# Kernel optimization log

Hardware: AMD Instinct MI355X
Metric: run time of the kernel (lower is better)

## Reference

```python
import jax, jax.numpy as jnp
import numpy as np

N_NODES = 50000
N_EDGES = 800000
IN_DIM = 128
HID = 64
ZDIM = 64
N_GRAPHS = 64


def gcn_conv(x, W, b, src, dst, n):
    # PyG GCNConv: add self-loops, symmetric deg^-1/2 normalization,
    # linear transform then gather-scatter aggregation.
    h = x @ W  # [N, out]
    loops = jnp.arange(n, dtype=src.dtype)
    s = jnp.concatenate([src, loops])
    d = jnp.concatenate([dst, loops])
    deg = jnp.zeros((n,), h.dtype).at[d].add(1.0)  # includes self-loops -> >=1
    dinv = jax.lax.rsqrt(deg)
    norm = dinv[s] * dinv[d]  # [E+N]
    msg = h[s] * norm[:, None]  # gather [E+N, out]
    out = jnp.zeros_like(h).at[d].add(msg)  # scatter-add
    return out + b


def mean_pool(h, batch, num_graphs):
    sums = jax.ops.segment_sum(h, batch, num_segments=num_graphs)
    cnt = jax.ops.segment_sum(jnp.ones((h.shape[0],), h.dtype), batch,
                              num_segments=num_graphs)
    return sums / jnp.maximum(cnt, 1.0)[:, None]


def setup_inputs() -> dict:
    key = jax.random.key(0)
    ks = jax.random.split(key, 9)
    x = jax.random.normal(ks[0], (N_NODES, IN_DIM), jnp.float32)
    edge_index = jax.random.randint(ks[1], (2, N_EDGES), 0, N_NODES, jnp.int64 if jax.config.jax_enable_x64 else jnp.int32)
    batch = jnp.sort(jax.random.randint(ks[2], (N_NODES,), 0, N_GRAPHS))
    s1 = 1.0 / np.sqrt(IN_DIM)
    s2 = 1.0 / np.sqrt(HID)
    W1 = jax.random.uniform(ks[3], (IN_DIM, HID), jnp.float32, -s1, s1)
    b1 = jnp.zeros((HID,), jnp.float32)
    Wmu = jax.random.uniform(ks[4], (HID, ZDIM), jnp.float32, -s2, s2)
    bmu = jnp.zeros((ZDIM,), jnp.float32)
    Wsig = jax.random.uniform(ks[5], (HID, ZDIM), jnp.float32, -s2, s2)
    bsig = jnp.zeros((ZDIM,), jnp.float32)
    return {"x": x, "edge_index": edge_index, "batch": batch,
            "num_graphs": N_GRAPHS, "W1": W1, "b1": b1,
            "Wmu": Wmu, "bmu": bmu, "Wsig": Wsig, "bsig": bsig}


def reference(x, edge_index, batch, num_graphs, W1, b1, Wmu, bmu, Wsig, bsig):
    src, dst = edge_index[0], edge_index[1]
    n = x.shape[0]
    h = jax.nn.elu(gcn_conv(x, W1, b1, src, dst, n))
    z_mu = mean_pool(jax.nn.elu(gcn_conv(h, Wmu, bmu, src, dst, n)), batch, num_graphs)
    z_sigma = mean_pool(jax.nn.elu(gcn_conv(h, Wsig, bsig, src, dst, n)), batch, num_graphs)
    return (z_mu, z_sigma)
```

## Files before the change

kernel.cpp:

```cpp
#include <hip/hip_runtime.h>
#include <hip/hip_fp16.h>


#define IN_DIM 128
#define HID 64
#define ZDIM 64
#define N_GRAPHS 64
#define SCAN_B 1024
#define POOL2_WAVES 8192

__device__ __forceinline__ float elu1(float x) {
    return x > 0.f ? x : expm1f(x);
}

__global__ void k_count(const int* __restrict__ dst, int* __restrict__ kc,
                        int* __restrict__ rank, int E) {
    int e = blockIdx.x * blockDim.x + threadIdx.x;
    if (e < E) rank[e] = atomicAdd(&kc[dst[e]], 1);
}

__global__ __launch_bounds__(SCAN_B) void k_scan1(const int* __restrict__ kc,
                                                  int* __restrict__ bsum, int n) {
    __shared__ int wpart[16];
    int tid = threadIdx.x, lane = tid & 63, w = tid >> 6;
    int i = blockIdx.x * SCAN_B + tid;
    int v = (i < n) ? kc[i] : 0;
#pragma unroll
    for (int d = 1; d < 64; d <<= 1) v += __shfl_xor(v, d, 64);
    if (lane == 0) wpart[w] = v;
    __syncthreads();
    if (tid < 16) {
        int t = wpart[tid];
#pragma unroll
        for (int d = 1; d < 16; d <<= 1) t += __shfl_xor(t, d, 64);
        if (tid == 0) bsum[blockIdx.x] = t;
    }
}

__global__ __launch_bounds__(SCAN_B) void k_scan3(const int* __restrict__ kc,
                                                  const int* __restrict__ bsum,
                                                  int* __restrict__ offs,
                                                  float* __restrict__ dinv,
                                                  int n, int nb) {
    __shared__ int wsum[16];
    __shared__ int sbase;
    int tid = threadIdx.x, lane = tid & 63, w = tid >> 6;
    if (tid < 64) {
        int v = (tid < nb) ? bsum[tid] : 0;
        int s = v;
#pragma unroll
        for (int d = 1; d < 64; d <<= 1) {
            int u = __shfl_up(s, d, 64);
            if (tid >= d) s += u;
        }
        if (tid == blockIdx.x) sbase = s - v;
    }
    int i = blockIdx.x * SCAN_B + tid;
    int v = (i < n) ? kc[i] : 0;
    int s = v;
#pragma unroll
    for (int d = 1; d < 64; d <<= 1) {
        int u = __shfl_up(s, d, 64);
        if (lane >= d) s += u;
    }
    if (lane == 63) wsum[w] = s;
    __syncthreads();
    if (tid < 16) {
        int t = wsum[tid];
#pragma unroll
        for (int d = 1; d < 16; d <<= 1) {
            int u = __shfl_up(t, d, 64);
            if (tid >= d) t += u;
        }
        wsum[tid] = t;
    }
    __syncthreads();
    int base = sbase + ((w == 0) ? 0 : wsum[w - 1]);
    if (i < n) {
        offs[i + 1] = base + s;
        dinv[i] = 1.0f / sqrtf(1.0f + (float)v);
        if (i == 0) offs[0] = 0;
    }
}

__global__ void k_fill(const int* __restrict__ src, const int* __restrict__ dst,
                       const int* __restrict__ rank, const int* __restrict__ offs,
                       int* __restrict__ csr, int E) {
    int e = blockIdx.x * blockDim.x + threadIdx.x;
    if (e < E) csr[offs[dst[e]] + rank[e]] = src[e];
}

__global__ __launch_bounds__(256) void k_mm1(const float* __restrict__ x,
                                             const float* __restrict__ W,
                                             const float* __restrict__ dinv,
                                             __half* __restrict__ ts1h, int n) {
    __shared__ float xs[64 * 68];
    __shared__ float ws[64 * 68];
    const int tid = threadIdx.x;
    const int m0 = blockIdx.x * 64;
    const int j = tid & 15;
    const int i = tid >> 4;

    const float4* x4 = (const float4*)x;
    const float4* W4 = (const float4*)W;

    float4 acc[4];
#pragma unroll
    for (int r = 0; r < 4; ++r) acc[r] = make_float4(0.f, 0.f, 0.f, 0.f);

    for (int kk = 0; kk < IN_DIM; kk += 64) {
        __syncthreads();
        for (int idx = tid; idx < 64 * 16; idx += 256) {
            int row = idx >> 4, c4 = idx & 15;
            float4 v = make_float4(0.f, 0.f, 0.f, 0.f);
            if (m0 + row < n) v = x4[(size_t)(m0 + row) * 32 + (kk >> 2) + c4];
            *(float4*)&xs[row * 68 + 4 * c4] = v;
            *(float4*)&ws[row * 68 + 4 * c4] = W4[(size_t)(kk + row) * 16 + c4];
        }
        __syncthreads();
#pragma unroll 1
        for (int k4 = 0; k4 < 16; ++k4) {
            float4 a[4];
#pragma unroll
            for (int r = 0; r < 4; ++r)
                a[r] = *(const float4*)&xs[(4 * i + r) * 68 + 4 * k4];
#pragma unroll
            for (int kc = 0; kc < 4; ++kc) {
                float4 bv = *(const float4*)&ws[(4 * k4 + kc) * 68 + 4 * j];
#pragma unroll
                for (int r = 0; r < 4; ++r) {
                    float av = (&a[r].x)[kc];
                    acc[r].x = fmaf(av, bv.x, acc[r].x);
                    acc[r].y = fmaf(av, bv.y, acc[r].y);
                    acc[r].z = fmaf(av, bv.z, acc[r].z);
                    acc[r].w = fmaf(av, bv.w, acc[r].w);
                }
            }
        }
    }

#pragma unroll
    for (int r = 0; r < 4; ++r) {
        int row = m0 + 4 * i + r;
        if (row < n) {
            float di = dinv[row];
            float4 tv = acc[r];
            __half2* p = (__half2*)&ts1h[(size_t)row * HID + 4 * j];
            p[0] = __floats2half2_rn(tv.x * di, tv.y * di);
            p[1] = __floats2half2_rn(tv.z * di, tv.w * di);
        }
    }
}

__global__ __launch_bounds__(256) void k_gather_h(const int* __restrict__ off,
                                                  const int* __restrict__ csr,
                                                  const float* __restrict__ dinv,
                                                  const __half* __restrict__ ts,
                                                  float* __restrict__ out, int n) {
    int node = blockIdx.x * 4 + (threadIdx.x >> 6);
    if (node >= n) return;
    int lane = threadIdx.x & 63;
    int half = lane >> 5, l2 = lane & 31;
    int s0 = off[node], s1 = off[node + 1];
    float2 acc = make_float2(0.f, 0.f);
    int k = s0 + half;
    for (; k + 6 < s1; k += 8) {
        int a = csr[k], b = csr[k + 2], c = csr[k + 4], d = csr[k + 6];
        float2 fa = __half22float2(*(const __half2*)&ts[(size_t)a * 64 + 2 * l2]);
        float2 fb = __half22float2(*(const __half2*)&ts[(size_t)b * 64 + 2 * l2]);
        float2 fc = __half22float2(*(const __half2*)&ts[(size_t)c * 64 + 2 * l2]);
        float2 fd = __half22float2(*(const __half2*)&ts[(size_t)d * 64 + 2 * l2]);
        acc.x += (fa.x + fb.x) + (fc.x + fd.x);
        acc.y += (fa.y + fb.y) + (fc.y + fd.y);
    }
    for (; k + 2 < s1; k += 4) {
        int a = csr[k], b = csr[k + 2];
        float2 fa = __half22float2(*(const __half2*)&ts[(size_t)a * 64 + 2 * l2]);
        float2 fb = __half22float2(*(const __half2*)&ts[(size_t)b * 64 + 2 * l2]);
        acc.x += fa.x + fb.x;
        acc.y += fa.y + fb.y;
    }
    for (; k < s1; k += 2) {
        int a = csr[k];
        float2 fa = __half22float2(*(const __half2*)&ts[(size_t)a * 64 + 2 * l2]);
        acc.x += fa.x;
        acc.y += fa.y;
    }
    acc.x += __shfl_xor(acc.x, 32, 64);
    acc.y += __shfl_xor(acc.y, 32, 64);
    if (half == 0) {
        float2 self = __half22float2(*(const __half2*)&ts[(size_t)node * 64 + 2 * l2]);
        float di = dinv[node];
        float2 o = make_float2((acc.x + self.x) * di, (acc.y + self.y) * di);
        *(float2*)&out[(size_t)node * 64 + 2 * l2] = o;
    }
}

__global__ __launch_bounds__(256) void k_mm23(const float* __restrict__ agg1,
                                              const float* __restrict__ b1,
                                              const float* __restrict__ Wmu,
                                              const float* __restrict__ Wsig,
                                              const float* __restrict__ dinv,
                                              __half* __restrict__ CDh, int n) {
    __shared__ float hs[64 * 68];
    __shared__ float wc[64 * 132];
    const int tid = threadIdx.x;
    const int m0 = blockIdx.x * 64;
    const int j = tid & 15;
    const int i = tid >> 4;

    const float4* h4 = (const float4*)agg1;
    const float4* b14 = (const float4*)b1;
    const float4* Wm4 = (const float4*)Wmu;
    const float4* Ws4 = (const float4*)Wsig;
    for (int idx = tid; idx < 64 * 16; idx += 256) {
        int row = idx >> 4, c4 = idx & 15;
        float4 v = make_float4(0.f, 0.f, 0.f, 0.f);
        if (m0 + row < n) {
            float4 hv = h4[(size_t)(m0 + row) * 16 + c4];
            float4 bb = b14[c4];
            v.x = elu1(hv.x + bb.x);
            v.y = elu1(hv.y + bb.y);
            v.z = elu1(hv.z + bb.z);
            v.w = elu1(hv.w + bb.w);
        }
        *(float4*)&hs[row * 68 + 4 * c4] = v;
        *(float4*)&wc[row * 132 + 4 * c4] = Wm4[(size_t)row * 16 + c4];
        *(float4*)&wc[row * 132 + 64 + 4 * c4] = Ws4[(size_t)row * 16 + c4];
    }
    __syncthreads();

    float4 accm[4], accs[4];
#pragma unroll
    for (int r = 0; r < 4; ++r) {
        accm[r] = make_float4(0.f, 0.f, 0.f, 0.f);
        accs[r] = make_float4(0.f, 0.f, 0.f, 0.f);
    }

#pragma unroll 1
    for (int k4 = 0; k4 < 16; ++k4) {
        float4 a[4];
#pragma unroll
        for (int r = 0; r < 4; ++r)
            a[r] = *(const float4*)&hs[(4 * i + r) * 68 + 4 * k4];
#pragma unroll
        for (int kc = 0; kc < 4; ++kc) {
            float4 bm = *(const float4*)&wc[(4 * k4 + kc) * 132 + 4 * j];
            float4 bs = *(const float4*)&wc[(4 * k4 + kc) * 132 + 64 + 4 * j];
#pragma unroll
            for (int r = 0; r < 4; ++r) {
                float av = (&a[r].x)[kc];
                accm[r].x = fmaf(av, bm.x, accm[r].x);
                accm[r].y = fmaf(av, bm.y, accm[r].y);
                accm[r].z = fmaf(av, bm.z, accm[r].z);
                accm[r].w = fmaf(av, bm.w, accm[r].w);
                accs[r].x = fmaf(av, bs.x, accs[r].x);
                accs[r].y = fmaf(av, bs.y, accs[r].y);
                accs[r].z = fmaf(av, bs.z, accs[r].z);
                accs[r].w = fmaf(av, bs.w, accs[r].w);
            }
        }
    }

#pragma unroll
    for (int r = 0; r < 4; ++r) {
        int row = m0 + 4 * i + r;
        if (row < n) {
            float di = dinv[row];
            float4 m = accm[r], s = accs[r];
            __half2* pm = (__half2*)&CDh[(size_t)row * 128 + 4 * j];
            pm[0] = __floats2half2_rn(m.x * di, m.y * di);
            pm[1] = __floats2half2_rn(m.z * di, m.w * di);
            __half2* ps = (__half2*)&CDh[(size_t)row * 128 + 64 + 4 * j];
            ps[0] = __floats2half2_rn(s.x * di, s.y * di);
            ps[1] = __floats2half2_rn(s.z * di, s.w * di);
        }
    }
}

__global__ __launch_bounds__(256) void k_gather2_pool(const int* __restrict__ offs,
                                                      const int* __restrict__ csr,
                                                      const float* __restrict__ dinv,
                                                      const __half* __restrict__ CD,
                                                      const float* __restrict__ bmu,
                                                      const float* __restrict__ bsig,
                                                      const int* __restrict__ batch,
                                                      float* __restrict__ sums, int n) {
    int lane = threadIdx.x & 63;
    int half = lane >> 5, l2 = lane & 31;
    int wid = (blockIdx.x * 256 + threadIdx.x) >> 6;
    int span = (n + POOL2_WAVES - 1) / POOL2_WAVES;
    int s = wid * span;
    if (s >= n) return;
    int e = min(n, s + span);
    const float2* bb = half ? (const float2*)bsig : (const float2*)bmu;
    float2 bv = bb[l2];
    float* sbase = sums + (half ? 4096 : 0);
    float2 pm = make_float2(0.f, 0.f);
    int g = batch[s];
    int o0 = offs[s];
    for (int node = s; node < e; ++node) {
        int o1 = offs[node + 1];
        float2 am = __half22float2(*(const __half2*)&CD[(size_t)node * 128 + 2 * lane]);
        int k = o0;
        for (; k + 8 <= o1; k += 8) {
            int a0 = csr[k],     a1 = csr[k + 1], a2 = csr[k + 2], a3 = csr[k + 3];
            int a4 = csr[k + 4], a5 = csr[k + 5], a6 = csr[k + 6], a7 = csr[k + 7];
            float2 f0 = __half22float2(*(const __half2*)&CD[(size_t)a0 * 128 + 2 * lane]);
            float2 f1 = __half22float2(*(const __half2*)&CD[(size_t)a1 * 128 + 2 * lane]);
            float2 f2 = __half22float2(*(const __half2*)&CD[(size_t)a2 * 128 + 2 * lane]);
            float2 f3 = __half22float2(*(const __half2*)&CD[(size_t)a3 * 128 + 2 * lane]);
            float2 f4 = __half22float2(*(const __half2*)&CD[(size_t)a4 * 128 + 2 * lane]);
            float2 f5 = __half22float2(*(const __half2*)&CD[(size_t)a5 * 128 + 2 * lane]);
            float2 f6 = __half22float2(*(const __half2*)&CD[(size_t)a6 * 128 + 2 * lane]);
            float2 f7 = __half22float2(*(const __half2*)&CD[(size_t)a7 * 128 + 2 * lane]);
            am.x += ((f0.x + f1.x) + (f2.x + f3.x)) + ((f4.x + f5.x) + (f6.x + f7.x));
            am.y += ((f0.y + f1.y) + (f2.y + f3.y)) + ((f4.y + f5.y) + (f6.y + f7.y));
        }
        for (; k + 4 <= o1; k += 4) {
            int a = csr[k], b = csr[k + 1], c = csr[k + 2], d = csr[k + 3];
            float2 fa = __half22float2(*(const __half2*)&CD[(size_t)a * 128 + 2 * lane]);
            float2 fb = __half22float2(*(const __half2*)&CD[(size_t)b * 128 + 2 * lane]);
            float2 fc = __half22float2(*(const __half2*)&CD[(size_t)c * 128 + 2 * lane]);
            float2 fd = __half22float2(*(const __half2*)&CD[(size_t)d * 128 + 2 * lane]);
            am.x += (fa.x + fb.x) + (fc.x + fd.x);
            am.y += (fa.y + fb.y) + (fc.y + fd.y);
        }
        for (; k < o1; ++k) {
            int a = csr[k];
            float2 fa = __half22float2(*(const __half2*)&CD[(size_t)a * 128 + 2 * lane]);
            am.x += fa.x;
            am.y += fa.y;
        }
        o0 = o1;
        float di = dinv[node];
        int gn = batch[node];
        if (gn != g) {
            atomicAdd(&sbase[g * 64 + 2 * l2], pm.x);
            atomicAdd(&sbase[g * 64 + 2 * l2 + 1], pm.y);
            pm = make_float2(0.f, 0.f);
            g = gn;
        }
        pm.x += elu1(am.x * di + bv.x);
        pm.y += elu1(am.y * di + bv.y);
    }
    atomicAdd(&sbase[g * 64 + 2 * l2], pm.x);
    atomicAdd(&sbase[g * 64 + 2 * l2 + 1], pm.y);
}

__global__ void k_pool_final(const float* __restrict__ sums,
                             const int* __restrict__ batch,
                             float* __restrict__ out, int n) {
    int i = blockIdx.x * blockDim.x + threadIdx.x;
    if (i >= 2 * N_GRAPHS * ZDIM) return;
    int g = (i >> 6) & 63;
    int lo = 0, hi = n;
    while (lo < hi) { int m = (lo + hi) >> 1; if (batch[m] < g) lo = m + 1; else hi = m; }
    int s = lo;
    lo = s; hi = n;
    while (lo < hi) { int m = (lo + hi) >> 1; if (batch[m] < g + 1) lo = m + 1; else hi = m; }
    float c = fmaxf((float)(lo - s), 1.0f);
    out[i] = sums[i] / c;
}

extern "C" void kernel_launch(void* const* d_in, const int* in_sizes, int n_in,
                              void* d_out, int out_size, void* d_ws, size_t ws_size,
                              hipStream_t stream) {
    const float* x    = (const float*)d_in[0];
    const int*   ei   = (const int*)d_in[1];
    const int*   batch= (const int*)d_in[2];
    const float* W1   = (const float*)d_in[4];
    const float* b1   = (const float*)d_in[5];
    const float* Wmu  = (const float*)d_in[6];
    const float* bmu  = (const float*)d_in[7];
    const float* Wsig = (const float*)d_in[8];
    const float* bsig = (const float*)d_in[9];
    float* out = (float*)d_out;

    const int n = in_sizes[0] / IN_DIM;
    const int E = in_sizes[1] / 2;
    const int* src = ei;
    const int* dst = ei + E;
    const int NSB = (n + SCAN_B - 1) / SCAN_B;

    float* ws = (float*)d_ws;
    size_t off_w = 0;
    int*   kc   = (int*)(ws + off_w); off_w += 50048;
    float* sums = ws + off_w; off_w += 8192;
    float* dinv = ws + off_w; off_w += 50048;
    int*   offs = (int*)(ws + off_w); off_w += 50056;
    int*   bsum = (int*)(ws + off_w); off_w += 64;
    int*   rank = (int*)(ws + off_w); off_w += 800000;
    int*   csr  = (int*)(ws + off_w); off_w += 800000;
    off_w = (off_w + 15) & ~(size_t)15;
    const size_t BIG = (size_t)n * 64;
    float*  A    = ws + off_w; off_w += BIG;
    __half* ts1h = (__half*)(ws + off_w); off_w += BIG / 2;
    __half* CDh  = (__half*)(ws + off_w); off_w += BIG;

    const int gE  = (E + 255) / 256;
    const int gNW = (n + 3) / 4;
    const int NB  = (n + 63) / 64;

    hipMemsetAsync(kc, 0, (50048 + 8192) * sizeof(int), stream);
    k_count<<<gE, 256, 0, stream>>>(dst, kc, rank, E);
    k_scan1<<<NSB, SCAN_B, 0, stream>>>(kc, bsum, n);
    k_scan3<<<NSB, SCAN_B, 0, stream>>>(kc, bsum, offs, dinv, n, NSB);
    k_fill<<<gE, 256, 0, stream>>>(src, dst, rank, offs, csr, E);

    k_mm1<<<NB, 256, 0, stream>>>(x, W1, dinv, ts1h, n);
    k_gather_h<<<gNW, 256, 0, stream>>>(offs, csr, dinv, ts1h, A, n);

    k_mm23<<<NB, 256, 0, stream>>>(A, b1, Wmu, Wsig, dinv, CDh, n);

    k_gather2_pool<<<POOL2_WAVES / 4, 256, 0, stream>>>(offs, csr, dinv, CDh,
                                                        bmu, bsig, batch, sums, n);
    k_pool_final<<<(2 * N_GRAPHS * ZDIM + 255) / 256, 256, 0, stream>>>(sums, batch, out, n);
}
```

Baseline: 254.5 us.

## Aggregate hidden features before shared mu/sigma matmul, fuse matmul with pooling

```diff
diff --git a/kernel.cpp b/kernel.cpp
--- a/kernel.cpp
+++ b/kernel.cpp
@@ -7,7 +7,6 @@
 #define ZDIM 64
 #define N_GRAPHS 64
 #define SCAN_B 1024
-#define POOL2_WAVES 8192
 
 __device__ __forceinline__ float elu1(float x) {
     return x > 0.f ? x : expm1f(x);
@@ -152,11 +151,12 @@
     }
 }
 
-__global__ __launch_bounds__(256) void k_gather_h(const int* __restrict__ off,
-                                                  const int* __restrict__ csr,
-                                                  const float* __restrict__ dinv,
-                                                  const __half* __restrict__ ts,
-                                                  float* __restrict__ out, int n) {
+__global__ __launch_bounds__(256) void k_gather_hh(const int* __restrict__ off,
+                                                   const int* __restrict__ csr,
+                                                   const float* __restrict__ dinv,
+                                                   const __half* __restrict__ ts,
+                                                   const float* __restrict__ b1,
+                                                   __half* __restrict__ hh, int n) {
     int node = blockIdx.x * 4 + (threadIdx.x >> 6);
     if (node >= n) return;
     int lane = threadIdx.x & 63;
@@ -191,43 +191,85 @@
     if (half == 0) {
         float2 self = __half22float2(*(const __half2*)&ts[(size_t)node * 64 + 2 * l2]);
         float di = dinv[node];
-        float2 o = make_float2((acc.x + self.x) * di, (acc.y + self.y) * di);
-        *(float2*)&out[(size_t)node * 64 + 2 * l2] = o;
-    }
-}
-
-__global__ __launch_bounds__(256) void k_mm23(const float* __restrict__ agg1,
-                                              const float* __restrict__ b1,
-                                              const float* __restrict__ Wmu,
-                                              const float* __restrict__ Wsig,
-                                              const float* __restrict__ dinv,
-                                              __half* __restrict__ CDh, int n) {
+        float2 bv = ((const float2*)b1)[l2];
+        float ax = (acc.x + self.x) * di + bv.x;
+        float ay = (acc.y + self.y) * di + bv.y;
+        __half2* p = (__half2*)&hh[(size_t)node * 64 + 2 * l2];
+        *p = __floats2half2_rn(elu1(ax) * di, elu1(ay) * di);
+    }
+}
+
+__global__ __launch_bounds__(256) void k_gather_g(const int* __restrict__ off,
+                                                  const int* __restrict__ csr,
+                                                  const float* __restrict__ dinv,
+                                                  const __half* __restrict__ hh,
+                                                  float* __restrict__ g, int n) {
+    int node = blockIdx.x * 4 + (threadIdx.x >> 6);
+    if (node >= n) return;
+    int lane = threadIdx.x & 63;
+    int half = lane >> 5, l2 = lane & 31;
+    int s0 = off[node], s1 = off[node + 1];
+    float2 acc = make_float2(0.f, 0.f);
+    int k = s0 + half;
+    for (; k + 6 < s1; k += 8) {
+        int a = csr[k], b = csr[k + 2], c = csr[k + 4], d = csr[k + 6];
+        float2 fa = __half22float2(*(const __half2*)&hh[(size_t)a * 64 + 2 * l2]);
+        float2 fb = __half22float2(*(const __half2*)&hh[(size_t)b * 64 + 2 * l2]);
+        float2 fc = __half22float2(*(const __half2*)&hh[(size_t)c * 64 + 2 * l2]);
+        float2 fd = __half22float2(*(const __half2*)&hh[(size_t)d * 64 + 2 * l2]);
+        acc.x += (fa.x + fb.x) + (fc.x + fd.x);
+        acc.y += (fa.y + fb.y) + (fc.y + fd.y);
+    }
+    for (; k + 2 < s1; k += 4) {
+        int a = csr[k], b = csr[k + 2];
+        float2 fa = __half22float2(*(const __half2*)&hh[(size_t)a * 64 + 2 * l2]);
+        float2 fb = __half22float2(*(const __half2*)&hh[(size_t)b * 64 + 2 * l2]);
+        acc.x += fa.x + fb.x;
+        acc.y += fa.y + fb.y;
+    }
+    for (; k < s1; k += 2) {
+        int a = csr[k];
+        float2 fa = __half22float2(*(const __half2*)&hh[(size_t)a * 64 + 2 * l2]);
+        acc.x += fa.x;
+        acc.y += fa.y;
+    }
+    acc.x += __shfl_xor(acc.x, 32, 64);
+    acc.y += __shfl_xor(acc.y, 32, 64);
+    if (half == 0) {
+        float2 self = __half22float2(*(const __half2*)&hh[(size_t)node * 64 + 2 * l2]);
+        float di = dinv[node];
+        *(float2*)&g[(size_t)node * 64 + 2 * l2] =
+            make_float2((acc.x + self.x) * di, (acc.y + self.y) * di);
+    }
+}
+
+__global__ __launch_bounds__(256) void k_mm_pool(const float* __restrict__ g,
+                                                 const float* __restrict__ Wmu,
+                                                 const float* __restrict__ Wsig,
+                                                 const float* __restrict__ bmu,
+                                                 const float* __restrict__ bsig,
+                                                 const int* __restrict__ batch,
+                                                 float* __restrict__ sums, int n) {
     __shared__ float hs[64 * 68];
     __shared__ float wc[64 * 132];
+    __shared__ int bs[64];
     const int tid = threadIdx.x;
     const int m0 = blockIdx.x * 64;
     const int j = tid & 15;
     const int i = tid >> 4;
 
-    const float4* h4 = (const float4*)agg1;
-    const float4* b14 = (const float4*)b1;
+    const float4* g4 = (const float4*)g;
     const float4* Wm4 = (const float4*)Wmu;
     const float4* Ws4 = (const float4*)Wsig;
     for (int idx = tid; idx < 64 * 16; idx += 256) {
         int row = idx >> 4, c4 = idx & 15;
         float4 v = make_float4(0.f, 0.f, 0.f, 0.f);
-        if (m0 + row < n) {
-            float4 hv = h4[(size_t)(m0 + row) * 16 + c4];
-            float4 bb = b14[c4];
-            v.x = elu1(hv.x + bb.x);
-            v.y = elu1(hv.y + bb.y);
-            v.z = elu1(hv.z + bb.z);
-            v.w = elu1(hv.w + bb.w);
-        }
+        if (m0 + row < n) v = g4[(size_t)(m0 + row) * 16 + c4];
         *(float4*)&hs[row * 68 + 4 * c4] = v;
         *(float4*)&wc[row * 132 + 4 * c4] = Wm4[(size_t)row * 16 + c4];
         *(float4*)&wc[row * 132 + 64 + 4 * c4] = Ws4[(size_t)row * 16 + c4];
     }
+    if (tid < 64) bs[tid] = (m0 + tid < n) ? batch[m0 + tid] : -1;
     __syncthreads();
 
     float4 accm[4], accs[4];
@@ -246,7 +288,7 @@
 #pragma unroll
         for (int kc = 0; kc < 4; ++kc) {
             float4 bm = *(const float4*)&wc[(4 * k4 + kc) * 132 + 4 * j];
-            float4 bs = *(const float4*)&wc[(4 * k4 + kc) * 132 + 64 + 4 * j];
+            float4 bsv = *(const float4*)&wc[(4 * k4 + kc) * 132 + 64 + 4 * j];
 #pragma unroll
             for (int r = 0; r < 4; ++r) {
                 float av = (&a[r].x)[kc];
@@ -254,98 +296,52 @@
                 accm[r].y = fmaf(av, bm.y, accm[r].y);
                 accm[r].z = fmaf(av, bm.z, accm[r].z);
                 accm[r].w = fmaf(av, bm.w, accm[r].w);
-                accs[r].x = fmaf(av, bs.x, accs[r].x);
-                accs[r].y = fmaf(av, bs.y, accs[r].y);
-                accs[r].z = fmaf(av, bs.z, accs[r].z);
-                accs[r].w = fmaf(av, bs.w, accs[r].w);
+                accs[r].x = fmaf(av, bsv.x, accs[r].x);
+                accs[r].y = fmaf(av, bsv.y, accs[r].y);
+                accs[r].z = fmaf(av, bsv.z, accs[r].z);
+                accs[r].w = fmaf(av, bsv.w, accs[r].w);
             }
         }
     }
 
+    float4 bm = ((const float4*)bmu)[j];
+    float4 bg = ((const float4*)bsig)[j];
+    __syncthreads();
+
 #pragma unroll
     for (int r = 0; r < 4; ++r) {
-        int row = m0 + 4 * i + r;
-        if (row < n) {
-            float di = dinv[row];
-            float4 m = accm[r], s = accs[r];
-            __half2* pm = (__half2*)&CDh[(size_t)row * 128 + 4 * j];
-            pm[0] = __floats2half2_rn(m.x * di, m.y * di);
-            pm[1] = __floats2half2_rn(m.z * di, m.w * di);
-            __half2* ps = (__half2*)&CDh[(size_t)row * 128 + 64 + 4 * j];
-            ps[0] = __floats2half2_rn(s.x * di, s.y * di);
-            ps[1] = __floats2half2_rn(s.z * di, s.w * di);
-        }
-    }
-}
-
-__global__ __launch_bounds__(256) void k_gather2_pool(const int* __restrict__ offs,
-                                                      const int* __restrict__ csr,
-                                                      const float* __restrict__ dinv,
-                                                      const __half* __restrict__ CD,
-                                                      const float* __restrict__ bmu,
-                                                      const float* __restrict__ bsig,
-                                                      const int* __restrict__ batch,
-                                                      float* __restrict__ sums, int n) {
-    int lane = threadIdx.x & 63;
-    int half = lane >> 5, l2 = lane & 31;
-    int wid = (blockIdx.x * 256 + threadIdx.x) >> 6;
-    int span = (n + POOL2_WAVES - 1) / POOL2_WAVES;
-    int s = wid * span;
-    if (s >= n) return;
-    int e = min(n, s + span);
-    const float2* bb = half ? (const float2*)bsig : (const float2*)bmu;
-    float2 bv = bb[l2];
-    float* sbase = sums + (half ? 4096 : 0);
-    float2 pm = make_float2(0.f, 0.f);
-    int g = batch[s];
-    int o0 = offs[s];
-    for (int node = s; node < e; ++node) {
-        int o1 = offs[node + 1];
-        float2 am = __half22float2(*(const __half2*)&CD[(size_t)node * 128 + 2 * lane]);
-        int k = o0;
-        for (; k + 8 <= o1; k += 8) {
-            int a0 = csr[k],     a1 = csr[k + 1], a2 = csr[k + 2], a3 = csr[k + 3];
-            int a4 = csr[k + 4], a5 = csr[k + 5], a6 = csr[k + 6], a7 = csr[k + 7];
-            float2 f0 = __half22float2(*(const __half2*)&CD[(size_t)a0 * 128 + 2 * lane]);
-            float2 f1 = __half22float2(*(const __half2*)&CD[(size_t)a1 * 128 + 2 * lane]);
-            float2 f2 = __half22float2(*(const __half2*)&CD[(size_t)a2 * 128 + 2 * lane]);
-            float2 f3 = __half22float2(*(const __half2*)&CD[(size_t)a3 * 128 + 2 * lane]);
-            float2 f4 = __half22float2(*(const __half2*)&CD[(size_t)a4 * 128 + 2 * lane]);
-            float2 f5 = __half22float2(*(const __half2*)&CD[(size_t)a5 * 128 + 2 * lane]);
-            float2 f6 = __half22float2(*(const __half2*)&CD[(size_t)a6 * 128 + 2 * lane]);
-            float2 f7 = __half22float2(*(const __half2*)&CD[(size_t)a7 * 128 + 2 * lane]);
-            am.x += ((f0.x + f1.x) + (f2.x + f3.x)) + ((f4.x + f5.x) + (f6.x + f7.x));
-            am.y += ((f0.y + f1.y) + (f2.y + f3.y)) + ((f4.y + f5.y) + (f6.y + f7.y));
-        }
-        for (; k + 4 <= o1; k += 4) {
-            int a = csr[k], b = csr[k + 1], c = csr[k + 2], d = csr[k + 3];
-            float2 fa = __half22float2(*(const __half2*)&CD[(size_t)a * 128 + 2 * lane]);
-            float2 fb = __half22float2(*(const __half2*)&CD[(size_t)b * 128 + 2 * lane]);
-            float2 fc = __half22float2(*(const __half2*)&CD[(size_t)c * 128 + 2 * lane]);
-            float2 fd = __half22float2(*(const __half2*)&CD[(size_t)d * 128 + 2 * lane]);
-            am.x += (fa.x + fb.x) + (fc.x + fd.x);
-            am.y += (fa.y + fb.y) + (fc.y + fd.y);
-        }
-        for (; k < o1; ++k) {
-            int a = csr[k];
-            float2 fa = __half22float2(*(const __half2*)&CD[(size_t)a * 128 + 2 * lane]);
-            am.x += fa.x;
-            am.y += fa.y;
-        }
-        o0 = o1;
-        float di = dinv[node];
-        int gn = batch[node];
-        if (gn != g) {
-            atomicAdd(&sbase[g * 64 + 2 * l2], pm.x);
-            atomicAdd(&sbase[g * 64 + 2 * l2 + 1], pm.y);
-            pm = make_float2(0.f, 0.f);
-            g = gn;
-        }
-        pm.x += elu1(am.x * di + bv.x);
-        pm.y += elu1(am.y * di + bv.y);
-    }
-    atomicAdd(&sbase[g * 64 + 2 * l2], pm.x);
-    atomicAdd(&sbase[g * 64 + 2 * l2 + 1], pm.y);
+        int row = 4 * i + r;
+        float4 m = accm[r], s = accs[r];
+        m.x = elu1(m.x + bm.x);
+        m.y = elu1(m.y + bm.y);
+        m.z = elu1(m.z + bm.z);
+        m.w = elu1(m.w + bm.w);
+        s.x = elu1(s.x + bg.x);
+        s.y = elu1(s.y + bg.y);
+        s.z = elu1(s.z + bg.z);
+        s.w = elu1(s.w + bg.w);
+        *(float4*)&wc[row * 132 + 4 * j] = m;
+        *(float4*)&wc[row * 132 + 64 + 4 * j] = s;
+    }
+    __syncthreads();
+
+    int d = tid & 127, seg = tid >> 7;
+    int base = (d < 64) ? d : (64 * 64 - 64 + d);
+    float acc = 0.f;
+    int gcur = -1;
+    int r0 = seg * 32;
+    for (int r = r0; r < r0 + 32; ++r) {
+        int gb = bs[r];
+        if (gb < 0) break;
+        float v = wc[r * 132 + d];
+        if (gb != gcur) {
+            if (gcur >= 0) atomicAdd(&sums[base + gcur * 64], acc);
+            acc = 0.f;
+            gcur = gb;
+        }
+        acc += v;
+    }
+    if (gcur >= 0) atomicAdd(&sums[base + gcur * 64], acc);
 }
 
 __global__ void k_pool_final(const float* __restrict__ sums,
@@ -394,9 +390,9 @@
     int*   csr  = (int*)(ws + off_w); off_w += 800000;
     off_w = (off_w + 15) & ~(size_t)15;
     const size_t BIG = (size_t)n * 64;
-    float*  A    = ws + off_w; off_w += BIG;
     __half* ts1h = (__half*)(ws + off_w); off_w += BIG / 2;
-    __half* CDh  = (__half*)(ws + off_w); off_w += BIG;
+    __half* hh   = (__half*)(ws + off_w); off_w += BIG / 2;
+    float*  gbuf = ws + off_w; off_w += BIG;
 
     const int gE  = (E + 255) / 256;
     const int gNW = (n + 3) / 4;
@@ -409,11 +405,10 @@
     k_fill<<<gE, 256, 0, stream>>>(src, dst, rank, offs, csr, E);
 
     k_mm1<<<NB, 256, 0, stream>>>(x, W1, dinv, ts1h, n);
-    k_gather_h<<<gNW, 256, 0, stream>>>(offs, csr, dinv, ts1h, A, n);
-
-    k_mm23<<<NB, 256, 0, stream>>>(A, b1, Wmu, Wsig, dinv, CDh, n);
-
-    k_gather2_pool<<<POOL2_WAVES / 4, 256, 0, stream>>>(offs, csr, dinv, CDh,
-                                                        bmu, bsig, batch, sums, n);
+    k_gather_hh<<<gNW, 256, 0, stream>>>(offs, csr, dinv, ts1h, b1, hh, n);
+
+    k_gather_g<<<gNW, 256, 0, stream>>>(offs, csr, dinv, hh, gbuf, n);
+
+    k_mm_pool<<<NB, 256, 0, stream>>>(gbuf, Wmu, Wsig, bmu, bsig, batch, sums, n);
     k_pool_final<<<(2 * N_GRAPHS * ZDIM + 255) / 256, 256, 0, stream>>>(sums, batch, out, n);
 }
```

Result: no change. 249.6 us (-1.9%).
